# Optimization experiments

Measured on AMD Instinct MI355X. Metric: run time of the kernel, lower is better.

## Reference

```python
import jax, jax.numpy as jnp
from jax import lax
import numpy as np

T, B, I, H = 512, 512, 128, 128
EPS = 1e-4


def setup_inputs() -> dict:
    key = jax.random.key(0)
    ks = jax.random.split(key, 8)
    s = 1.0 / np.sqrt(H)
    x = jax.random.normal(ks[0], (T, B, I), dtype=jnp.float32)
    gt = jax.random.bernoulli(ks[1], 0.5, (T, B, 1)).astype(jnp.float32)
    W_ih = jax.random.uniform(ks[2], (3 * H, I), jnp.float32, -s, s)
    W_hh = jax.random.uniform(ks[3], (3 * H, H), jnp.float32, -s, s)
    b_ih = jax.random.uniform(ks[4], (3 * H,), jnp.float32, -s, s)
    b_hh = jax.random.uniform(ks[5], (3 * H,), jnp.float32, -s, s)
    W_dec = jax.random.uniform(ks[6], (1, H), jnp.float32, -s, s)
    b_dec = jax.random.uniform(ks[7], (1,), jnp.float32, -s, s)
    return {"x": x, "gt": gt, "W_ih": W_ih, "W_hh": W_hh, "b_ih": b_ih,
            "b_hh": b_hh, "W_dec": W_dec, "b_dec": b_dec}


def reference(x, gt, W_ih, W_hh, b_ih, b_hh, W_dec, b_dec):
    # Precompute input-side gate projections for all steps: [T, B, 3H]
    xp = jnp.einsum('tbi,gi->tbg', x, W_ih) + b_ih

    def step(carry, inp):
        h, acc = carry
        xpt, gtt = inp  # xpt: [B,3H], gtt: [B,1]
        hp = h @ W_hh.T + b_hh  # [B,3H]
        xr, xz, xn = jnp.split(xpt, 3, axis=-1)
        hr, hz, hn = jnp.split(hp, 3, axis=-1)
        r = jax.nn.sigmoid(xr + hr)
        z = jax.nn.sigmoid(xz + hz)
        n = jnp.tanh(xn + r * hn)
        h_new = (1.0 - z) * n + z * h
        C = jax.nn.sigmoid(h_new @ W_dec.T + b_dec)  # [B,1]
        nll = -jnp.sum(gtt * jnp.log(C + EPS) + (1.0 - gtt) * jnp.log(1.0 - C + EPS))
        return (h_new, acc + nll), None

    h0 = jnp.zeros((x.shape[1], W_hh.shape[1]), x.dtype)
    # loop t = 0 .. T-2: uses x[t] and gt[t+1]
    (_, nll), _ = lax.scan(step, (h0, jnp.zeros((), x.dtype)), (xp[:-1], gt[1:]))
    return nll / np.float32(gt.size)
```

## Files before the change

kernel.cpp:

```cpp
#include <hip/hip_runtime.h>
#include <stdint.h>

#define B_DIM 512
#define I_DIM 128
#define H_DIM 128
#define NSTEP 511

typedef __attribute__((ext_vector_type(4))) float f32x4;
typedef _Float16 half2_t __attribute__((ext_vector_type(2)));
typedef _Float16 half8_t __attribute__((ext_vector_type(8)));

#define BAR_LDS() asm volatile("s_waitcnt lgkmcnt(0)\n\ts_barrier" ::: "memory")
#define MFMA16(A, B, C) __builtin_amdgcn_mfma_f32_16x16x32_f16(A, B, C, 0, 0, 0)

__device__ __forceinline__ float frcp(float v) {
#if __has_builtin(__builtin_amdgcn_rcpf)
  return __builtin_amdgcn_rcpf(v);
#else
  return 1.f / v;
#endif
}
__device__ __forceinline__ unsigned pkrtz_u(float a, float b) {
#if __has_builtin(__builtin_amdgcn_cvt_pkrtz)
  return __builtin_bit_cast(unsigned, __builtin_amdgcn_cvt_pkrtz(a, b));
#else
  half2_t r; r.x = (_Float16)a; r.y = (_Float16)b;
  return __builtin_bit_cast(unsigned, r);
#endif
}
__device__ __forceinline__ uint2 pack_f32x4(f32x4 v) {
  uint2 p;
  p.x = pkrtz_u(v[0], v[1]);
  p.y = pkrtz_u(v[2], v[3]);
  return p;
}
__device__ __forceinline__ f32x4 unpack_u2(uint2 v) {
  const half2_t a = __builtin_bit_cast(half2_t, v.x);
  const half2_t b = __builtin_bit_cast(half2_t, v.y);
  return (f32x4){(float)a.x, (float)a.y, (float)b.x, (float)b.y};
}

__global__ __launch_bounds__(768, 3) void k_rec(
    const float* __restrict__ x, const float* __restrict__ gt,
    const float* __restrict__ Wih, const float* __restrict__ Whh,
    const float* __restrict__ bih, const float* __restrict__ bhh,
    const float* __restrict__ Wdec, const float* __restrict__ bdec,
    float* __restrict__ nll_part) {
  __shared__ __align__(16) _Float16 hT[2][16 * 128];
  __shared__ __align__(16) _Float16 xT[2][16 * 128];
  __shared__ __align__(16) uint2 pp[2][3][4][128];
  __shared__ float gl[NSTEP * 16];

  const int tid = threadIdx.x;
  const int lane = tid & 63;
  const int w = tid >> 6;
  const int l15 = lane & 15, l4 = lane >> 4;
  const int row0 = blockIdx.x * 16;

#pragma unroll
  for (int q = 0; q < 11; ++q) {
    const int idx = tid + 768 * q;
    if (idx < NSTEP * 16)
      gl[idx] = gt[(size_t)((idx >> 4) + 1) * B_DIM + row0 + (idx & 15)];
  }

  if (w < 8) {
    const int u = 16 * w + l15;

    half8_t bh[3][4];
#pragma unroll
    for (int g3 = 0; g3 < 3; ++g3)
#pragma unroll
      for (int ks = 0; ks < 4; ++ks) {
        const size_t off = (size_t)(g3 * H_DIM + u) * H_DIM + ks * 32 + l4 * 8;
        const float4 a = *(const float4*)(Whh + off);
        const float4 b = *(const float4*)(Whh + off + 4);
        half8_t v;
        v[0] = (_Float16)a.x; v[1] = (_Float16)a.y;
        v[2] = (_Float16)a.z; v[3] = (_Float16)a.w;
        v[4] = (_Float16)b.x; v[5] = (_Float16)b.y;
        v[6] = (_Float16)b.z; v[7] = (_Float16)b.w;
        bh[g3][ks] = v;
      }
    half8_t wdB[4];
#pragma unroll
    for (int ks = 0; ks < 4; ++ks) {
      half8_t v;
#pragma unroll
      for (int j = 0; j < 8; ++j)
        v[j] = (l15 == 0) ? (_Float16)Wdec[ks * 32 + l4 * 8 + j] : (_Float16)0.f;
      wdB[ks] = v;
    }
    const float bhn = bhh[2 * H_DIM + u];
    const float bd0 = bdec[0];
    const f32x4 cN = (f32x4){bhn, bhn, bhn, bhn};

    *(uint2*)((char*)hT[0] + tid * 8) = (uint2){0u, 0u};

    float h_old[4] = {0.f, 0.f, 0.f, 0.f};
    float nllA[4] = {0.f, 0.f, 0.f, 0.f};
    __syncthreads();
    __syncthreads();

#pragma unroll 1
    for (int i = 0; i < NSTEP; ++i) {
      const char* hb = (const char*)hT[i & 1];
      half8_t ah[4];
#pragma unroll
      for (int ks = 0; ks < 4; ++ks)
        ah[ks] = *(const half8_t*)(hb + l15 * 256 +
                                   ((((ks << 2) | l4) ^ l15) << 4));
      f32x4 aR = unpack_u2(pp[i & 1][0][l4][u]);
      f32x4 aZ = unpack_u2(pp[i & 1][1][l4][u]);
      const f32x4 pN = unpack_u2(pp[i & 1][2][l4][u]);
      f32x4 aN = cN;
#pragma unroll
      for (int ks = 0; ks < 4; ++ks) {
        aR = MFMA16(ah[ks], bh[0][ks], aR);
        aZ = MFMA16(ah[ks], bh[1][ks], aZ);
        aN = MFMA16(ah[ks], bh[2][ks], aN);
      }

      if (w == 0 && i > 0) {
        f32x4 aD = (f32x4){0.f, 0.f, 0.f, 0.f};
#pragma unroll
        for (int ks = 0; ks < 4; ++ks) aD = MFMA16(ah[ks], wdB[ks], aD);
        if (l15 == 0) {
#pragma unroll
          for (int r = 0; r < 4; ++r) {
            const float C = frcp(1.f + __expf(-(aD[r] + bd0)));
            const float g = gl[(i - 1) * 16 + 4 * l4 + r];
            nllA[r] -= g * __logf(C + 1e-4f) +
                       (1.f - g) * __logf(1.f - C + 1e-4f);
          }
        }
      }

      char* hw = (char*)hT[(i + 1) & 1];
#pragma unroll
      for (int r = 0; r < 4; ++r) {
        const float r_ = frcp(1.f + __expf(-aR[r]));
        const float z_ = frcp(1.f + __expf(-aZ[r]));
        const float a2 = pN[r] + r_ * aN[r];
        const float n_ = 1.f - 2.f * frcp(__expf(2.f * a2) + 1.f);
        const float hnew = n_ + z_ * (h_old[r] - n_);
        h_old[r] = hnew;
        const int b = 4 * l4 + r;
        *(_Float16*)(hw + b * 256 + (((u >> 3) ^ b) << 4) + (u & 7) * 2) =
            (_Float16)hnew;
      }
      BAR_LDS();
    }

    if (w == 0) {
      const char* hb = (const char*)hT[NSTEP & 1];
      half8_t ah[4];
#pragma unroll
      for (int ks = 0; ks < 4; ++ks)
        ah[ks] = *(const half8_t*)(hb + l15 * 256 +
                                   ((((ks << 2) | l4) ^ l15) << 4));
      f32x4 aD = (f32x4){0.f, 0.f, 0.f, 0.f};
#pragma unroll
      for (int ks = 0; ks < 4; ++ks) aD = MFMA16(ah[ks], wdB[ks], aD);
      if (l15 == 0) {
#pragma unroll
        for (int r = 0; r < 4; ++r) {
          const float C = frcp(1.f + __expf(-(aD[r] + bd0)));
          const float g = gl[(NSTEP - 1) * 16 + 4 * l4 + r];
          nllA[r] -= g * __logf(C + 1e-4f) +
                     (1.f - g) * __logf(1.f - C + 1e-4f);
          nll_part[row0 + 4 * l4 + r] = nllA[r];
        }
      }
    }
  } else {
    const int wx = w - 8;
    const int u0 = 32 * wx + l15;

    half8_t bx[2][3][4];
    float brz0[2], brz1[2], bxn[2];
#pragma unroll
    for (int c = 0; c < 2; ++c) {
      const int u = u0 + 16 * c;
#pragma unroll
      for (int g3 = 0; g3 < 3; ++g3)
#pragma unroll
        for (int ks = 0; ks < 4; ++ks) {
          const size_t off =
              (size_t)(g3 * H_DIM + u) * H_DIM + ks * 32 + l4 * 8;
          const float4 a = *(const float4*)(Wih + off);
          const float4 b = *(const float4*)(Wih + off + 4);
          half8_t v;
          v[0] = (_Float16)a.x; v[1] = (_Float16)a.y;
          v[2] = (_Float16)a.z; v[3] = (_Float16)a.w;
          v[4] = (_Float16)b.x; v[5] = (_Float16)b.y;
          v[6] = (_Float16)b.z; v[7] = (_Float16)b.w;
          bx[c][g3][ks] = v;
        }
      brz0[c] = bih[u] + bhh[u];
      brz1[c] = bih[H_DIM + u] + bhh[H_DIM + u];
      bxn[c] = bih[2 * H_DIM + u];
    }

    const int xt = tid - 512;
    const int sxr = xt >> 4;
    const int c16 = xt & 15;
    const int sbyte = sxr * 256 + ((c16 ^ sxr) << 4);
    const size_t xlbase = ((size_t)row0 + sxr) * I_DIM + c16 * 8;

    {
#pragma unroll
      for (int t = 0; t < 2; ++t) {
        const float4 v0 = *(const float4*)&x[(size_t)t * B_DIM * I_DIM + xlbase];
        const float4 v1 =
            *(const float4*)&x[(size_t)t * B_DIM * I_DIM + xlbase + 4];
        uint4 p;
        p.x = pkrtz_u(v0.x, v0.y);
        p.y = pkrtz_u(v0.z, v0.w);
        p.z = pkrtz_u(v1.x, v1.y);
        p.w = pkrtz_u(v1.z, v1.w);
        *(uint4*)((char*)xT[t] + sbyte) = p;
      }
    }
    float4 xA0 = *(const float4*)&x[(size_t)2 * B_DIM * I_DIM + xlbase];
    float4 xA1 = *(const float4*)&x[(size_t)2 * B_DIM * I_DIM + xlbase + 4];
    __syncthreads();

    {
      const char* xb = (const char*)xT[0];
      half8_t af[4];
#pragma unroll
      for (int ks = 0; ks < 4; ++ks)
        af[ks] = *(const half8_t*)(xb + l15 * 256 +
                                   ((((ks << 2) | l4) ^ l15) << 4));
#pragma unroll
      for (int c = 0; c < 2; ++c) {
        f32x4 aR = (f32x4){brz0[c], brz0[c], brz0[c], brz0[c]};
        f32x4 aZ = (f32x4){brz1[c], brz1[c], brz1[c], brz1[c]};
        f32x4 aN = (f32x4){bxn[c], bxn[c], bxn[c], bxn[c]};
#pragma unroll
        for (int ks = 0; ks < 4; ++ks) {
          aR = MFMA16(af[ks], bx[c][0][ks], aR);
          aZ = MFMA16(af[ks], bx[c][1][ks], aZ);
          aN = MFMA16(af[ks], bx[c][2][ks], aN);
        }
        pp[0][0][l4][u0 + 16 * c] = pack_f32x4(aR);
        pp[0][1][l4][u0 + 16 * c] = pack_f32x4(aZ);
        pp[0][2][l4][u0 + 16 * c] = pack_f32x4(aN);
      }
    }
    __syncthreads();

#pragma unroll 1
    for (int i = 0; i < NSTEP; ++i) {
      const char* xb = (const char*)xT[(i + 1) & 1];
      half8_t af[4];
#pragma unroll
      for (int ks = 0; ks < 4; ++ks)
        af[ks] = *(const half8_t*)(xb + l15 * 256 +
                                   ((((ks << 2) | l4) ^ l15) << 4));
#pragma unroll
      for (int c = 0; c < 2; ++c) {
        f32x4 aR = (f32x4){brz0[c], brz0[c], brz0[c], brz0[c]};
        f32x4 aZ = (f32x4){brz1[c], brz1[c], brz1[c], brz1[c]};
        f32x4 aN = (f32x4){bxn[c], bxn[c], bxn[c], bxn[c]};
#pragma unroll
        for (int ks = 0; ks < 4; ++ks) {
          aR = MFMA16(af[ks], bx[c][0][ks], aR);
          aZ = MFMA16(af[ks], bx[c][1][ks], aZ);
          aN = MFMA16(af[ks], bx[c][2][ks], aN);
        }
        pp[(i + 1) & 1][0][l4][u0 + 16 * c] = pack_f32x4(aR);
        pp[(i + 1) & 1][1][l4][u0 + 16 * c] = pack_f32x4(aZ);
        pp[(i + 1) & 1][2][l4][u0 + 16 * c] = pack_f32x4(aN);
      }

      {
        uint4 p;
        p.x = pkrtz_u(xA0.x, xA0.y);
        p.y = pkrtz_u(xA0.z, xA0.w);
        p.z = pkrtz_u(xA1.x, xA1.y);
        p.w = pkrtz_u(xA1.z, xA1.w);
        *(uint4*)((char*)xT[i & 1] + sbyte) = p;
        const size_t trow =
            (size_t)((i + 3 < 512) ? i + 3 : 511) * B_DIM * I_DIM;
        xA0 = *(const float4*)&x[trow + xlbase];
        xA1 = *(const float4*)&x[trow + xlbase + 4];
      }
      BAR_LDS();
    }
  }
}

__global__ __launch_bounds__(512) void k_fin(const float* __restrict__ nll_part,
                                             float* __restrict__ out) {
  __shared__ float red[8];
  const int tid = threadIdx.x;
  float v = nll_part[tid];
#pragma unroll
  for (int off = 32; off; off >>= 1) v += __shfl_down(v, off);
  if ((tid & 63) == 0) red[tid >> 6] = v;
  __syncthreads();
  if (tid == 0) {
    float s = 0.f;
#pragma unroll
    for (int i = 0; i < 8; ++i) s += red[i];
    out[0] = s * (1.f / (512.f * 512.f));
  }
}

extern "C" void kernel_launch(void* const* d_in, const int* in_sizes, int n_in,
                              void* d_out, int out_size, void* d_ws,
                              size_t ws_size, hipStream_t stream) {
  const float* x    = (const float*)d_in[0];
  const float* gt   = (const float*)d_in[1];
  const float* Wih  = (const float*)d_in[2];
  const float* Whh  = (const float*)d_in[3];
  const float* bih  = (const float*)d_in[4];
  const float* bhh  = (const float*)d_in[5];
  const float* Wdec = (const float*)d_in[6];
  const float* bdec = (const float*)d_in[7];

  float* nll_part = (float*)d_ws;

  k_rec<<<dim3(32), dim3(768), 0, stream>>>(
      x, gt, Wih, Whh, bih, bhh, Wdec, bdec, nll_part);
  k_fin<<<dim3(1), dim3(512), 0, stream>>>(nll_part, (float*)d_out);
}
```

Before: 519.3 us.

## Move decoder NLL into a dedicated wave and add input projections after MFMA

Adds a 13th wavefront that computes the decoder logit and NLL accumulation each step, taking that work off wave 0 of the recurrent gate group so the critical path of the recurrence is no longer lengthened by wave 0's extra MFMAs and transcendentals. The recurrent MFMAs now start from zero accumulators instead of the unpacked input projections, and the projections are added afterwards, so the LDS reads and unpacks can overlap the MFMA chain. The cost is a larger block (832 threads), an extra wave taking part in every barrier, and a launch bound changed to one block per CU.

Measured after the change: 925.8 us. +78.3%, slower.

```diff
diff --git a/kernel.cpp b/kernel.cpp
--- a/kernel.cpp
+++ b/kernel.cpp
@@ -40,7 +40,7 @@
   return (f32x4){(float)a.x, (float)a.y, (float)b.x, (float)b.y};
 }
 
-__global__ __launch_bounds__(768, 3) void k_rec(
+__global__ __launch_bounds__(832, 1) void k_rec(
     const float* __restrict__ x, const float* __restrict__ gt,
     const float* __restrict__ Wih, const float* __restrict__ Whh,
     const float* __restrict__ bih, const float* __restrict__ bhh,
@@ -58,8 +58,8 @@
   const int row0 = blockIdx.x * 16;
 
 #pragma unroll
-  for (int q = 0; q < 11; ++q) {
-    const int idx = tid + 768 * q;
+  for (int q = 0; q < 10; ++q) {
+    const int idx = tid + 832 * q;
     if (idx < NSTEP * 16)
       gl[idx] = gt[(size_t)((idx >> 4) + 1) * B_DIM + row0 + (idx & 15)];
   }
@@ -82,23 +82,13 @@
         v[6] = (_Float16)b.z; v[7] = (_Float16)b.w;
         bh[g3][ks] = v;
       }
-    half8_t wdB[4];
-#pragma unroll
-    for (int ks = 0; ks < 4; ++ks) {
-      half8_t v;
-#pragma unroll
-      for (int j = 0; j < 8; ++j)
-        v[j] = (l15 == 0) ? (_Float16)Wdec[ks * 32 + l4 * 8 + j] : (_Float16)0.f;
-      wdB[ks] = v;
-    }
     const float bhn = bhh[2 * H_DIM + u];
-    const float bd0 = bdec[0];
     const f32x4 cN = (f32x4){bhn, bhn, bhn, bhn};
+    const f32x4 c0 = (f32x4){0.f, 0.f, 0.f, 0.f};
 
     *(uint2*)((char*)hT[0] + tid * 8) = (uint2){0u, 0u};
 
     float h_old[4] = {0.f, 0.f, 0.f, 0.f};
-    float nllA[4] = {0.f, 0.f, 0.f, 0.f};
     __syncthreads();
     __syncthreads();
 
@@ -110,37 +100,26 @@
       for (int ks = 0; ks < 4; ++ks)
         ah[ks] = *(const half8_t*)(hb + l15 * 256 +
                                    ((((ks << 2) | l4) ^ l15) << 4));
-      f32x4 aR = unpack_u2(pp[i & 1][0][l4][u]);
-      f32x4 aZ = unpack_u2(pp[i & 1][1][l4][u]);
-      const f32x4 pN = unpack_u2(pp[i & 1][2][l4][u]);
-      f32x4 aN = cN;
+      const uint2 puR = pp[i & 1][0][l4][u];
+      const uint2 puZ = pp[i & 1][1][l4][u];
+      const uint2 puN = pp[i & 1][2][l4][u];
+
+      f32x4 aR = c0, aZ = c0, aN = cN;
 #pragma unroll
       for (int ks = 0; ks < 4; ++ks) {
         aR = MFMA16(ah[ks], bh[0][ks], aR);
         aZ = MFMA16(ah[ks], bh[1][ks], aZ);
         aN = MFMA16(ah[ks], bh[2][ks], aN);
       }
-
-      if (w == 0 && i > 0) {
-        f32x4 aD = (f32x4){0.f, 0.f, 0.f, 0.f};
-#pragma unroll
-        for (int ks = 0; ks < 4; ++ks) aD = MFMA16(ah[ks], wdB[ks], aD);
-        if (l15 == 0) {
-#pragma unroll
-          for (int r = 0; r < 4; ++r) {
-            const float C = frcp(1.f + __expf(-(aD[r] + bd0)));
-            const float g = gl[(i - 1) * 16 + 4 * l4 + r];
-            nllA[r] -= g * __logf(C + 1e-4f) +
-                       (1.f - g) * __logf(1.f - C + 1e-4f);
-          }
-        }
-      }
+      const f32x4 pR = unpack_u2(puR);
+      const f32x4 pZ = unpack_u2(puZ);
+      const f32x4 pN = unpack_u2(puN);
 
       char* hw = (char*)hT[(i + 1) & 1];
 #pragma unroll
       for (int r = 0; r < 4; ++r) {
-        const float r_ = frcp(1.f + __expf(-aR[r]));
-        const float z_ = frcp(1.f + __expf(-aZ[r]));
+        const float r_ = frcp(1.f + __expf(-(aR[r] + pR[r])));
+        const float z_ = frcp(1.f + __expf(-(aZ[r] + pZ[r])));
         const float a2 = pN[r] + r_ * aN[r];
         const float n_ = 1.f - 2.f * frcp(__expf(2.f * a2) + 1.f);
         const float hnew = n_ + z_ * (h_old[r] - n_);
@@ -151,29 +130,7 @@
       }
       BAR_LDS();
     }
-
-    if (w == 0) {
-      const char* hb = (const char*)hT[NSTEP & 1];
-      half8_t ah[4];
-#pragma unroll
-      for (int ks = 0; ks < 4; ++ks)
-        ah[ks] = *(const half8_t*)(hb + l15 * 256 +
-                                   ((((ks << 2) | l4) ^ l15) << 4));
-      f32x4 aD = (f32x4){0.f, 0.f, 0.f, 0.f};
-#pragma unroll
-      for (int ks = 0; ks < 4; ++ks) aD = MFMA16(ah[ks], wdB[ks], aD);
-      if (l15 == 0) {
-#pragma unroll
-        for (int r = 0; r < 4; ++r) {
-          const float C = frcp(1.f + __expf(-(aD[r] + bd0)));
-          const float g = gl[(NSTEP - 1) * 16 + 4 * l4 + r];
-          nllA[r] -= g * __logf(C + 1e-4f) +
-                     (1.f - g) * __logf(1.f - C + 1e-4f);
-          nll_part[row0 + 4 * l4 + r] = nllA[r];
-        }
-      }
-    }
-  } else {
+  } else if (w < 12) {
     const int wx = w - 8;
     const int u0 = 32 * wx + l15;
 
@@ -289,6 +246,68 @@
       }
       BAR_LDS();
     }
+  } else {
+    half8_t wdB[4];
+#pragma unroll
+    for (int ks = 0; ks < 4; ++ks) {
+      half8_t v;
+#pragma unroll
+      for (int j = 0; j < 8; ++j)
+        v[j] = (l15 == 0) ? (_Float16)Wdec[ks * 32 + l4 * 8 + j] : (_Float16)0.f;
+      wdB[ks] = v;
+    }
+    const float bd0 = bdec[0];
+    float nllA[4] = {0.f, 0.f, 0.f, 0.f};
+
+    __syncthreads();
+    __syncthreads();
+
+#pragma unroll 1
+    for (int i = 0; i < NSTEP; ++i) {
+      if (i > 0) {
+        const char* hb = (const char*)hT[i & 1];
+        half8_t dh[4];
+#pragma unroll
+        for (int ks = 0; ks < 4; ++ks)
+          dh[ks] = *(const half8_t*)(hb + l15 * 256 +
+                                     ((((ks << 2) | l4) ^ l15) << 4));
+        f32x4 aD = (f32x4){0.f, 0.f, 0.f, 0.f};
+#pragma unroll
+        for (int ks = 0; ks < 4; ++ks) aD = MFMA16(dh[ks], wdB[ks], aD);
+        if (l15 == 0) {
+#pragma unroll
+          for (int r = 0; r < 4; ++r) {
+            const float C = frcp(1.f + __expf(-(aD[r] + bd0)));
+            const float g = gl[(i - 1) * 16 + 4 * l4 + r];
+            nllA[r] -= g * __logf(C + 1e-4f) +
+                       (1.f - g) * __logf(1.f - C + 1e-4f);
+          }
+        }
+      }
+      BAR_LDS();
+    }
+
+    {
+      const char* hb = (const char*)hT[NSTEP & 1];
+      half8_t dh[4];
+#pragma unroll
+      for (int ks = 0; ks < 4; ++ks)
+        dh[ks] = *(const half8_t*)(hb + l15 * 256 +
+                                   ((((ks << 2) | l4) ^ l15) << 4));
+      f32x4 aD = (f32x4){0.f, 0.f, 0.f, 0.f};
+#pragma unroll
+      for (int ks = 0; ks < 4; ++ks) aD = MFMA16(dh[ks], wdB[ks], aD);
+      if (l15 == 0) {
+#pragma unroll
+        for (int r = 0; r < 4; ++r) {
+          const float C = frcp(1.f + __expf(-(aD[r] + bd0)));
+          const float g = gl[(NSTEP - 1) * 16 + 4 * l4 + r];
+          nllA[r] -= g * __logf(C + 1e-4f) +
+                     (1.f - g) * __logf(1.f - C + 1e-4f);
+          nll_part[row0 + 4 * l4 + r] = nllA[r];
+        }
+      }
+    }
   }
 }
 
@@ -323,7 +342,7 @@
 
   float* nll_part = (float*)d_ws;
 
-  k_rec<<<dim3(32), dim3(768), 0, stream>>>(
+  k_rec<<<dim3(32), dim3(832), 0, stream>>>(
       x, gt, Wih, Whh, bih, bhh, Wdec, bdec, nll_part);
   k_fin<<<dim3(1), dim3(512), 0, stream>>>(nll_part, (float*)d_out);
 }
```
